# Kernel optimization log

Measured on AMD Instinct MI355X. Metric: run time of the kernel, lower is better.

Reference implementation:

```python
import jax, jax.numpy as jnp
import numpy as np

V_IPC, N_ROLES, D = 50000, 16, 256
B, L = 2048, 64
F_BIB, H1, H2, D_OUT = 512, 1024, 1024, 512
N_EXP, N_CLS = 8, 10
LN_EPS = 1e-5


def setup_inputs() -> dict:
    key = jax.random.key(0)
    ks = jax.random.split(key, 24)
    s = 0.05
    ipc_emb = jax.random.normal(ks[0], (V_IPC, D), jnp.float32) * s
    ipc_emb = ipc_emb.at[0].set(0.0)  # padding_idx=0
    role_emb = jax.random.normal(ks[1], (N_ROLES, D), jnp.float32) * s
    role_emb = role_emb.at[0].set(0.0)
    inp = {
        "ipc_indices": jax.random.randint(ks[2], (B, L), 0, V_IPC),
        "role_indices": jax.random.randint(ks[3], (B, L), 0, N_ROLES),
        "bibliometric_features": jax.random.normal(ks[4], (B, F_BIB), jnp.float32),
        "ipc_padding_mask": jax.random.randint(ks[5], (B, L), 0, 2).astype(jnp.int32),
        "top_k": 2,
        "ipc_emb": ipc_emb,
        "role_emb": role_emb,
        "Wq": jax.random.normal(ks[6], (D, D), jnp.float32) * s,
        "bq": jnp.zeros((D,), jnp.float32),
        "Wk": jax.random.normal(ks[7], (D, D), jnp.float32) * s,
        "bk": jnp.zeros((D,), jnp.float32),
        "Wv": jax.random.normal(ks[8], (D, D), jnp.float32) * s,
        "bv": jnp.zeros((D,), jnp.float32),
        "global_context": jax.random.normal(ks[9], (D,), jnp.float32) * s,
        "ln_g": jnp.ones((D,), jnp.float32),
        "ln_b": jnp.zeros((D,), jnp.float32),
        "gate_W": jax.random.normal(ks[10], (D, N_EXP), jnp.float32) * s,
        "gate_b": jnp.zeros((N_EXP,), jnp.float32),
        "expert_biases": jnp.zeros((N_EXP,), jnp.float32),
        "W1": jax.random.normal(ks[11], (N_EXP, F_BIB, H1), jnp.float32) * s,
        "b1": jnp.zeros((N_EXP, H1), jnp.float32),
        "W2": jax.random.normal(ks[12], (N_EXP, H1, H2), jnp.float32) * s,
        "b2": jnp.zeros((N_EXP, H2), jnp.float32),
        "W3": jax.random.normal(ks[13], (N_EXP, H2, D_OUT), jnp.float32) * s,
        "b3": jnp.zeros((N_EXP, D_OUT), jnp.float32),
        "head_W": jax.random.normal(ks[14], (D_OUT, N_CLS), jnp.float32) * s,
        "head_b": jnp.zeros((N_CLS,), jnp.float32),
    }
    return inp


def reference(ipc_indices, role_indices, bibliometric_features, ipc_padding_mask, top_k,
              ipc_emb, role_emb, Wq, bq, Wk, bk, Wv, bv, global_context, ln_g, ln_b,
              gate_W, gate_b, expert_biases, W1, b1, W2, b2, W3, b3, head_W, head_b):
    # embeddings + role combine  -> [B, L, D]
    x = ipc_emb[ipc_indices] + role_emb[role_indices]
    # attention pooling with a global learned query (same query for every batch row)
    keys = x @ Wk + bk                                  # [B, L, D]
    values = x @ Wv + bv                                # [B, L, D]
    q = global_context @ Wq + bq                        # [D]
    scores = jnp.einsum('d,bld->bl', q, keys)           # [B, L]
    scores = jnp.where(ipc_padding_mask == 0, -1e9, scores)
    attn = jax.nn.softmax(scores, axis=-1)              # [B, L]
    pooled = jnp.einsum('bl,bld->bd', attn, values)     # [B, D]
    mu = pooled.mean(-1, keepdims=True)
    var = ((pooled - mu) ** 2).mean(-1, keepdims=True)
    router_in = (pooled - mu) / jnp.sqrt(var + LN_EPS) * ln_g + ln_b
    # router: select with biased scores, gate with unbiased scores
    affinity = router_in @ gate_W + gate_b              # [B, E]
    sel_scores = affinity + expert_biases
    _, idx = jax.lax.top_k(sel_scores, top_k)           # [B, K]
    gw = jax.nn.softmax(jnp.take_along_axis(affinity, idx, axis=-1), axis=-1)  # [B, K]
    # dense all-expert MLP (reference form of masked per-expert loop)
    h = jax.nn.relu(jnp.einsum('bi,eih->ebh', bibliometric_features, W1) + b1[:, None, :])
    h = jax.nn.relu(jnp.einsum('ebh,ehj->ebj', h, W2) + b2[:, None, :])
    eo = jnp.einsum('ebj,ejo->ebo', h, W3) + b3[:, None, :]  # [E, B, O]
    # gather each token's top-k expert outputs and combine
    bidx = jnp.arange(idx.shape[0])[:, None]            # [B, 1]
    sel_out = eo[idx, bidx]                             # [B, K, O]
    moe_out = jnp.einsum('bk,bko->bo', gw, sel_out)     # [B, O]
    logits = moe_out @ head_W + head_b                  # [B, n_classes]
    return logits, idx
```

## Files before the change

### kernel.cpp

```cpp
#include <hip/hip_runtime.h>
#include <hip/hip_bf16.h>
#include <math.h>


#define LN_EPS 1e-5f

typedef __bf16 bf16_t;
typedef __bf16 bf16x8 __attribute__((ext_vector_type(8)));
typedef float f32x4 __attribute__((ext_vector_type(4)));

struct f4x2 { float4 a, b; };
__device__ __forceinline__ f4x2 ldA8(const float* p) {
  f4x2 v; v.a = *(const float4*)p; v.b = *(const float4*)(p + 4); return v;
}
__device__ __forceinline__ bf16x8 cvt8(const f4x2& v) {
  bf16x8 o;
  o[0] = (bf16_t)v.a.x; o[1] = (bf16_t)v.a.y; o[2] = (bf16_t)v.a.z; o[3] = (bf16_t)v.a.w;
  o[4] = (bf16_t)v.b.x; o[5] = (bf16_t)v.b.y; o[6] = (bf16_t)v.b.z; o[7] = (bf16_t)v.b.w;
  return o;
}

__global__ __launch_bounds__(256)
void prep_kq_kernel(const float* __restrict__ Wq, const float* __restrict__ bq,
                    const float* __restrict__ Wk, const float* __restrict__ bk,
                    const float* __restrict__ gc, float* __restrict__ kq_out) {
  __shared__ float q[256];
  __shared__ float red[4];
  const int t = threadIdx.x, bi = blockIdx.x;
  float s = bq[t];
  for (int d = 0; d < 256; d++) s += gc[d] * Wq[d * 256 + t];
  q[t] = s;
  __syncthreads();
  const int rl = t >> 5, sl = t & 31;
  const int r = bi * 8 + rl;
  float p = 0.f;
#pragma unroll
  for (int i = 0; i < 8; i++) { const int d = sl + 32 * i; p += Wk[r * 256 + d] * q[d]; }
#pragma unroll
  for (int o = 16; o > 0; o >>= 1) p += __shfl_down(p, o, 32);
  if (sl == 0) kq_out[r] = p;
  if (bi == 0) {
    float z2 = q[t] * bk[t];
    const int lane = t & 63, wave = t >> 6;
#pragma unroll
    for (int o = 32; o > 0; o >>= 1) z2 += __shfl_down(z2, o);
    if (lane == 0) red[wave] = z2;
    __syncthreads();
    if (t == 0) kq_out[256] = red[0] + red[1] + red[2] + red[3];
  }
}

__global__ __launch_bounds__(256)
void xbar_transpose(const float* __restrict__ W1, const float* __restrict__ W2,
                    const float* __restrict__ W3, bf16_t* __restrict__ B1,
                    bf16_t* __restrict__ B2, bf16_t* __restrict__ B3,
                    const int* __restrict__ ipc_idx, const int* __restrict__ role_idx,
                    const int* __restrict__ maskp,
                    const float* __restrict__ ipc_emb, const float* __restrict__ role_emb,
                    const float* __restrict__ kq_qbk, float* __restrict__ xbar_g) {
  __shared__ __align__(16) float smem[4480];
  const int bid = blockIdx.x;
  const int t = threadIdx.x, lane = t & 63;

  if (bid < 2048) {
    const int b = bid, wave = t >> 6;
    float* sred = smem;
    float* scores_s = smem + 4352;
    float* attn_s = smem + 4416;
    const float4 kq = *(const float4*)(kq_qbk + lane * 4);
    const float qbk = kq_qbk[256];
    const int rbase = b * 64 + wave * 16;
    int4 m4[4], i4[4], r4[4];
#pragma unroll
    for (int j = 0; j < 4; j++) {
      m4[j] = *(const int4*)(maskp + rbase + j * 4);
      i4[j] = *(const int4*)(ipc_idx + rbase + j * 4);
      r4[j] = *(const int4*)(role_idx + rbase + j * 4);
    }
#pragma unroll
    for (int i = 0; i < 16; i++) {
      const int mki = (&m4[i / 4].x)[i % 4];
      const int ii = mki ? (&i4[i / 4].x)[i % 4] : 0;
      const int ri = mki ? (&r4[i / 4].x)[i % 4] : 0;
      const float4 xe = *(const float4*)(ipc_emb + (size_t)ii * 256 + lane * 4);
      const float4 re = *(const float4*)(role_emb + (size_t)ri * 256 + lane * 4);
      sred[(wave * 64 + lane) * 17 + i] =
          (xe.x + re.x) * kq.x + (xe.y + re.y) * kq.y +
          (xe.z + re.z) * kq.z + (xe.w + re.w) * kq.w;
    }
    __syncthreads();
    {
      const int i_r = lane & 15, g = lane >> 4;
      float s = 0.f;
#pragma unroll
      for (int j = 0; j < 16; j++) s += sred[(wave * 64 + g * 16 + j) * 17 + i_r];
      s += __shfl_xor(s, 16);
      s += __shfl_xor(s, 32);
      const int mval = maskp[rbase + i_r];
      if (lane < 16) scores_s[wave * 16 + lane] = mval ? (s + qbk) : -1e9f;
    }
    __syncthreads();
    if (wave == 0) {
      const float sv = scores_s[lane];
      float m = sv;
#pragma unroll
      for (int o = 32; o > 0; o >>= 1) m = fmaxf(m, __shfl_xor(m, o));
      const float ev = expf(sv - m);
      float sum = ev;
#pragma unroll
      for (int o = 32; o > 0; o >>= 1) sum += __shfl_xor(sum, o);
      attn_s[lane] = ev / sum;
    }
    __syncthreads();
    float p0 = 0.f, p1 = 0.f, p2 = 0.f, p3 = 0.f;
#pragma unroll
    for (int i = 0; i < 16; i++) {
      const int mki = (&m4[i / 4].x)[i % 4];
      const int ii = mki ? (&i4[i / 4].x)[i % 4] : 0;
      const int ri = mki ? (&r4[i / 4].x)[i % 4] : 0;
      const float a = attn_s[wave * 16 + i];
      const float4 xe = *(const float4*)(ipc_emb + (size_t)ii * 256 + lane * 4);
      const float4 re = *(const float4*)(role_emb + (size_t)ri * 256 + lane * 4);
      p0 += a * (xe.x + re.x); p1 += a * (xe.y + re.y);
      p2 += a * (xe.z + re.z); p3 += a * (xe.w + re.w);
    }
    __syncthreads();
    *(float4*)&smem[wave * 256 + lane * 4] = make_float4(p0, p1, p2, p3);
    __syncthreads();
    xbar_g[(size_t)b * 256 + t] = smem[t] + smem[256 + t] + smem[512 + t] + smem[768 + t];
    return;
  }

  const int bid2 = bid - 2048;
  const float* W; bf16_t* Bft; int K, N, e, n0, k0;
  if (bid2 < 1024) {
    W = W1; Bft = B1; K = 512; N = 1024;
    e = bid2 >> 7; const int r = bid2 & 127;
    n0 = (r & 15) * 64; k0 = (r >> 4) * 64;
  } else if (bid2 < 3072) {
    W = W2; Bft = B2; K = 1024; N = 1024;
    const int q = bid2 - 1024; e = q >> 8; const int r = q & 255;
    n0 = (r & 15) * 64; k0 = (r >> 4) * 64;
  } else {
    W = W3; Bft = B3; K = 1024; N = 512;
    const int q = bid2 - 3072; e = q >> 7; const int r = q & 127;
    n0 = (r & 7) * 64; k0 = (r >> 3) * 64;
  }
  float (*tile)[65] = (float(*)[65])smem;
  const float* Wp = W + (size_t)e * K * N;
  bf16_t* Bp = Bft + (size_t)e * N * K;
  const int tq = t & 15, th = t >> 4;
#pragma unroll
  for (int i = 0; i < 4; i++) {
    const int row = th + 16 * i;
    *(float4*)&tile[row][tq * 4] = *(const float4*)(Wp + (size_t)(k0 + row) * N + n0 + tq * 4);
  }
  __syncthreads();
  const int sub = t >> 6;
  const int nk = K >> 5;
#pragma unroll
  for (int it = 0; it < 2; it++) {
    const int fid = sub + it * 4;
    const int ntl = fid & 3, ktl = fid >> 2;
    const int n_l = ntl * 16 + (lane & 15);
    const int k_l = ktl * 32 + (lane >> 4) * 8;
    bf16x8 o;
#pragma unroll
    for (int j = 0; j < 8; j++) o[j] = (bf16_t)tile[k_l + j][n_l];
    const size_t idx = ((((size_t)(n0 >> 4) + ntl) * nk + (k0 >> 5) + ktl) * 64 + lane) * 8;
    *(bf16x8*)(Bp + idx) = o;
  }
}

__global__ __launch_bounds__(256)
void pool_kernel(const float* __restrict__ xbar_g, const float* __restrict__ Wv,
                 const float* __restrict__ bvec,
                 const float* __restrict__ ln_g, const float* __restrict__ ln_b,
                 const float* __restrict__ gate_W, const float* __restrict__ gate_b,
                 const float* __restrict__ expert_biases,
                 float* __restrict__ out_idx_f, int* __restrict__ ws_idx,
                 float* __restrict__ ws_gw) {
  const int rb = blockIdx.x * 8;
  __shared__ __align__(16) float xs[8][256];
  __shared__ __align__(16) float pp[4][8][256];
  const int t = threadIdx.x, wave = t >> 6, lane = t & 63;
  for (int i = t; i < 512; i += 256)
    ((float4*)xs)[i] = ((const float4*)(xbar_g + (size_t)rb * 256))[i];
  __syncthreads();
  f32x4 acc[8];
#pragma unroll
  for (int r = 0; r < 8; r++) acc[r] = (f32x4){0.f, 0.f, 0.f, 0.f};
  const int dbase = wave * 64;
  for (int dd = 0; dd < 64; dd += 4) {
    float4 xr[8];
#pragma unroll
    for (int r = 0; r < 8; r++) xr[r] = *(const float4*)&xs[r][dbase + dd];
#pragma unroll
    for (int j = 0; j < 4; j++) {
      const float4 wv = *(const float4*)(Wv + (size_t)(dbase + dd + j) * 256 + lane * 4);
#pragma unroll
      for (int r = 0; r < 8; r++) {
        const float xv = (&xr[r].x)[j];
        acc[r][0] += xv * wv.x; acc[r][1] += xv * wv.y;
        acc[r][2] += xv * wv.z; acc[r][3] += xv * wv.w;
      }
    }
  }
#pragma unroll
  for (int r = 0; r < 8; r++) *(f32x4*)&pp[wave][r][lane * 4] = acc[r];
  __syncthreads();
  const float4 bvv = *(const float4*)(bvec + lane * 4);
  const float4 lg = *(const float4*)(ln_g + lane * 4);
  const float4 lb = *(const float4*)(ln_b + lane * 4);
#pragma unroll
  for (int rr = 0; rr < 2; rr++) {
    const int r = wave * 2 + rr;
    f32x4 v = *(const f32x4*)&pp[0][r][lane * 4];
#pragma unroll
    for (int w2 = 1; w2 < 4; w2++) {
      const f32x4 qv = *(const f32x4*)&pp[w2][r][lane * 4];
      v[0] += qv[0]; v[1] += qv[1]; v[2] += qv[2]; v[3] += qv[3];
    }
    v[0] += bvv.x; v[1] += bvv.y; v[2] += bvv.z; v[3] += bvv.w;
    float s1 = v[0] + v[1] + v[2] + v[3];
#pragma unroll
    for (int o = 32; o > 0; o >>= 1) s1 += __shfl_xor(s1, o);
    const float mu = s1 * (1.f / 256.f);
    const float4 df = make_float4(v[0] - mu, v[1] - mu, v[2] - mu, v[3] - mu);
    float s2 = df.x * df.x + df.y * df.y + df.z * df.z + df.w * df.w;
#pragma unroll
    for (int o = 32; o > 0; o >>= 1) s2 += __shfl_xor(s2, o);
    const float inv = 1.f / sqrtf(s2 * (1.f / 256.f) + LN_EPS);
    f32x4 rv;
    rv[0] = df.x * inv * lg.x + lb.x; rv[1] = df.y * inv * lg.y + lb.y;
    rv[2] = df.z * inv * lg.z + lb.z; rv[3] = df.w * inv * lg.w + lb.w;
    f32x4 pa = {0.f, 0.f, 0.f, 0.f}, pb = {0.f, 0.f, 0.f, 0.f};
#pragma unroll
    for (int k = 0; k < 4; k++) {
      const int d = lane * 4 + k;
      const f32x4 g0 = *(const f32x4*)(gate_W + d * 8);
      const f32x4 g1 = *(const f32x4*)(gate_W + d * 8 + 4);
      pa += rv[k] * g0;
      pb += rv[k] * g1;
    }
#pragma unroll
    for (int o = 32; o > 0; o >>= 1) {
      pa[0] += __shfl_down(pa[0], o); pa[1] += __shfl_down(pa[1], o);
      pa[2] += __shfl_down(pa[2], o); pa[3] += __shfl_down(pa[3], o);
      pb[0] += __shfl_down(pb[0], o); pb[1] += __shfl_down(pb[1], o);
      pb[2] += __shfl_down(pb[2], o); pb[3] += __shfl_down(pb[3], o);
    }
    if (lane == 0) {
      float aff[8];
#pragma unroll
      for (int j = 0; j < 4; j++) { aff[j] = pa[j] + gate_b[j]; aff[4 + j] = pb[j] + gate_b[4 + j]; }
      float b0 = -1e30f; int i0 = 0;
#pragma unroll
      for (int j = 0; j < 8; j++) {
        const float s = aff[j] + expert_biases[j];
        if (s > b0) { b0 = s; i0 = j; }
      }
      float b1v = -1e30f; int i1 = 0;
#pragma unroll
      for (int j = 0; j < 8; j++) {
        const float s = aff[j] + expert_biases[j];
        if (j != i0 && s > b1v) { b1v = s; i1 = j; }
      }
      const float a0 = aff[i0], a1 = aff[i1];
      const float m = fmaxf(a0, a1);
      const float e0 = expf(a0 - m), e1 = expf(a1 - m);
      const float invs = 1.f / (e0 + e1);
      const int bg = rb + r;
      ws_idx[bg * 2] = i0; ws_idx[bg * 2 + 1] = i1;
      ws_gw[bg * 2] = e0 * invs; ws_gw[bg * 2 + 1] = e1 * invs;
      out_idx_f[bg * 2] = (float)i0; out_idx_f[bg * 2 + 1] = (float)i1;
    }
  }
}

__global__ __launch_bounds__(256)
void pack_kernel(const int* __restrict__ ws_idx, int* __restrict__ list_token,
                 int* __restrict__ a_of, int* __restrict__ offsets_g) {
  __shared__ int cnt[8]; __shared__ int off[9]; __shared__ int fill[8];
  const int t = threadIdx.x;
  if (t < 8) cnt[t] = 0;
  __syncthreads();
  for (int a = t; a < 4096; a += 256) atomicAdd(&cnt[ws_idx[a]], 1);
  __syncthreads();
  if (t == 0) {
    off[0] = 0;
    for (int e = 0; e < 8; e++) off[e + 1] = off[e] + ((cnt[e] + 63) & ~63);
  }
  __syncthreads();
  if (t < 8) fill[t] = off[t];
  if (t < 9) offsets_g[t] = off[t];
  for (int a = t; a < 4608; a += 256) list_token[a] = 0;
  __syncthreads();
  for (int a = t; a < 4096; a += 256) {
    const int e = ws_idx[a];
    const int pos = atomicAdd(&fill[e], 1);
    list_token[pos] = a >> 1;
    a_of[a] = pos;
  }
}

template <int NT, bool RELU>
__global__ __launch_bounds__(256)
void expert_gemm_g1(const float* __restrict__ bib, const int* __restrict__ list_token,
                    const bf16_t* __restrict__ Bft, const float* __restrict__ bias,
                    bf16_t* __restrict__ C, const int* __restrict__ offsets) {
  constexpr int K = 512, nk = K / 32;
  const int e = blockIdx.z;
  const int seg_hi = offsets[e + 1];
  const int blk_row = offsets[e] + blockIdx.y * 128;
  if (blk_row >= seg_hi) return;
  const int wave = threadIdx.x >> 6, lane = threadIdx.x & 63;
  const int row0 = blk_row + wave * 32;
  if (row0 >= seg_hi) return;
  const int n0 = blockIdx.x * 64;
  const int tok0 = list_token[row0 + (lane & 15)];
  const int tok1 = list_token[row0 + 16 + (lane & 15)];
  const float* Ap0 = bib + (size_t)tok0 * 512 + (lane >> 4) * 8;
  const float* Ap1 = bib + (size_t)tok1 * 512 + (lane >> 4) * 8;
  const bf16_t* Bp = Bft + (size_t)e * NT * K + ((size_t)(n0 >> 4) * nk * 512 + lane * 8);
  f32x4 acc[2][4];
#pragma unroll
  for (int i = 0; i < 2; i++)
#pragma unroll
    for (int j = 0; j < 4; j++) acc[i][j] = (f32x4){0.f, 0.f, 0.f, 0.f};
  f4x2 aS[2][2]; bf16x8 bX[2][4];
  aS[0][0] = ldA8(Ap0); aS[0][1] = ldA8(Ap1);
#pragma unroll
  for (int ni = 0; ni < 4; ni++) bX[0][ni] = *(const bf16x8*)(Bp + (size_t)ni * nk * 512);
#pragma unroll
  for (int kt = 0; kt < nk; kt++) {
    const int cur = kt & 1, nxt = cur ^ 1;
    if (kt + 1 < nk) {
      aS[nxt][0] = ldA8(Ap0 + (kt + 1) * 32);
      aS[nxt][1] = ldA8(Ap1 + (kt + 1) * 32);
#pragma unroll
      for (int ni = 0; ni < 4; ni++)
        bX[nxt][ni] = *(const bf16x8*)(Bp + ((size_t)ni * nk + kt + 1) * 512);
    }
    const bf16x8 a0 = cvt8(aS[cur][0]), a1 = cvt8(aS[cur][1]);
#pragma unroll
    for (int ni = 0; ni < 4; ni++) {
      acc[0][ni] = __builtin_amdgcn_mfma_f32_16x16x32_bf16(a0, bX[cur][ni], acc[0][ni], 0, 0, 0);
      acc[1][ni] = __builtin_amdgcn_mfma_f32_16x16x32_bf16(a1, bX[cur][ni], acc[1][ni], 0, 0, 0);
    }
  }
  const int fr = lane & 15, q = lane >> 4;
#pragma unroll
  for (int ni = 0; ni < 4; ni++) {
    const int col = n0 + ni * 16 + fr;
    const float bv = bias[e * NT + col];
#pragma unroll
    for (int mi = 0; mi < 2; mi++) {
#pragma unroll
      for (int r = 0; r < 4; r++) {
        const int row = row0 + mi * 16 + q * 4 + r;
        float v = acc[mi][ni][r] + bv;
        if (RELU) v = fmaxf(v, 0.f);
        C[(size_t)row * NT + col] = (bf16_t)v;
      }
    }
  }
}

template <int K, int NT, bool RELU, typename OUT_T>
__global__ __launch_bounds__(256)
void expert_gemm_ft(const bf16_t* __restrict__ A, const bf16_t* __restrict__ Bft,
                    const float* __restrict__ bias, OUT_T* __restrict__ C,
                    const int* __restrict__ offsets) {
  constexpr int nk = K / 32;
  const int e = blockIdx.z;
  const int seg_hi = offsets[e + 1];
  const int blk_row = offsets[e] + blockIdx.y * 128;
  if (blk_row >= seg_hi) return;
  const int wave = threadIdx.x >> 6, lane = threadIdx.x & 63;
  const int row0 = blk_row + wave * 32;
  if (row0 >= seg_hi) return;
  const int n0 = blockIdx.x * 64;
  const bf16_t* Ap = A + (size_t)(row0 + (lane & 15)) * K + ((lane >> 4) * 8);
  const bf16_t* Bp = Bft + (size_t)e * NT * K + ((size_t)(n0 >> 4) * nk * 512 + lane * 8);
  f32x4 acc[2][4];
#pragma unroll
  for (int i = 0; i < 2; i++)
#pragma unroll
    for (int j = 0; j < 4; j++) acc[i][j] = (f32x4){0.f, 0.f, 0.f, 0.f};
  bf16x8 aX[2][2], bX[2][4];
#pragma unroll
  for (int mi = 0; mi < 2; mi++) aX[0][mi] = *(const bf16x8*)(Ap + mi * 16 * K);
#pragma unroll
  for (int ni = 0; ni < 4; ni++) bX[0][ni] = *(const bf16x8*)(Bp + (size_t)ni * nk * 512);
#pragma unroll
  for (int kt = 0; kt < nk; kt++) {
    const int cur = kt & 1, nxt = cur ^ 1;
    if (kt + 1 < nk) {
#pragma unroll
      for (int mi = 0; mi < 2; mi++)
        aX[nxt][mi] = *(const bf16x8*)(Ap + mi * 16 * K + (kt + 1) * 32);
#pragma unroll
      for (int ni = 0; ni < 4; ni++)
        bX[nxt][ni] = *(const bf16x8*)(Bp + ((size_t)ni * nk + kt + 1) * 512);
    }
#pragma unroll
    for (int mi = 0; mi < 2; mi++)
#pragma unroll
      for (int ni = 0; ni < 4; ni++)
        acc[mi][ni] = __builtin_amdgcn_mfma_f32_16x16x32_bf16(aX[cur][mi], bX[cur][ni], acc[mi][ni], 0, 0, 0);
  }
  const int fr = lane & 15, q = lane >> 4;
#pragma unroll
  for (int ni = 0; ni < 4; ni++) {
    const int col = n0 + ni * 16 + fr;
    const float bv = bias[e * NT + col];
#pragma unroll
    for (int mi = 0; mi < 2; mi++) {
#pragma unroll
      for (int r = 0; r < 4; r++) {
        const int row = row0 + mi * 16 + q * 4 + r;
        float v = acc[mi][ni][r] + bv;
        if (RELU) v = fmaxf(v, 0.f);
        C[(size_t)row * NT + col] = (OUT_T)v;
      }
    }
  }
}

__global__ __launch_bounds__(256)
void head_kernel(const float* __restrict__ O, const int* __restrict__ a_of,
                 const float* __restrict__ ws_gw, const float* __restrict__ head_W,
                 const float* __restrict__ head_b, float* __restrict__ out) {
  const int b = blockIdx.x, t = threadIdx.x;
  __shared__ float m[512];
  const int a0 = a_of[b * 2], a1 = a_of[b * 2 + 1];
  const float g0 = ws_gw[b * 2], g1 = ws_gw[b * 2 + 1];
  for (int d = t; d < 512; d += 256)
    m[d] = g0 * O[(size_t)a0 * 512 + d] + g1 * O[(size_t)a1 * 512 + d];
  __syncthreads();
  if (t < 160) {
    const int c = t >> 4, ch = t & 15;
    float p = 0.f;
#pragma unroll
    for (int i = 0; i < 32; i++) {
      const int d = i * 16 + ch;
      p += m[d] * head_W[d * 10 + c];
    }
#pragma unroll
    for (int o = 8; o > 0; o >>= 1) p += __shfl_down(p, o, 16);
    if (ch == 0) out[b * 10 + c] = p + head_b[c];
  }
}

extern "C" void kernel_launch(void* const* d_in, const int* in_sizes, int n_in,
                              void* d_out, int out_size, void* d_ws, size_t ws_size,
                              hipStream_t stream) {
  const int* ipc_idx = (const int*)d_in[0];
  const int* role_idx = (const int*)d_in[1];
  const float* bib = (const float*)d_in[2];
  const int* maskp = (const int*)d_in[3];
  const float* ipc_emb = (const float*)d_in[5];
  const float* role_emb = (const float*)d_in[6];
  const float* Wq = (const float*)d_in[7];
  const float* bq = (const float*)d_in[8];
  const float* Wk = (const float*)d_in[9];
  const float* bk = (const float*)d_in[10];
  const float* Wv = (const float*)d_in[11];
  const float* bv = (const float*)d_in[12];
  const float* gc = (const float*)d_in[13];
  const float* ln_g = (const float*)d_in[14];
  const float* ln_b = (const float*)d_in[15];
  const float* gate_W = (const float*)d_in[16];
  const float* gate_b = (const float*)d_in[17];
  const float* exp_b = (const float*)d_in[18];
  const float* W1 = (const float*)d_in[19];
  const float* b1 = (const float*)d_in[20];
  const float* W2 = (const float*)d_in[21];
  const float* b2 = (const float*)d_in[22];
  const float* W3 = (const float*)d_in[23];
  const float* b3 = (const float*)d_in[24];
  const float* head_W = (const float*)d_in[25];
  const float* head_b = (const float*)d_in[26];

  char* ws = (char*)d_ws;
  size_t off = 0;
  auto alloc = [&](size_t bytes) -> char* {
    char* p = ws + off;
    off += (bytes + 255) & ~(size_t)255;
    return p;
  };
  float* kq_qbk = (float*)alloc(257 * 4);
  float* xbar_g = (float*)alloc((size_t)2048 * 256 * 4);
  int* ws_idx = (int*)alloc(4096 * 4);
  float* ws_gw = (float*)alloc(4096 * 4);
  int* list_tok = (int*)alloc(4608 * 4);
  int* a_of = (int*)alloc(4096 * 4);
  int* offs = (int*)alloc(9 * 4);
  bf16_t* W1t = (bf16_t*)alloc((size_t)8 * 1024 * 512 * 2);
  bf16_t* W2t = (bf16_t*)alloc((size_t)8 * 1024 * 1024 * 2);
  bf16_t* W3t = (bf16_t*)alloc((size_t)8 * 512 * 1024 * 2);
  bf16_t* H1c = (bf16_t*)alloc((size_t)4608 * 1024 * 2);
  bf16_t* H2c = (bf16_t*)alloc((size_t)4608 * 1024 * 2);
  float* Oc = (float*)alloc((size_t)4608 * 512 * 4);
  (void)in_sizes; (void)n_in; (void)out_size; (void)ws_size;

  float* out_logits = (float*)d_out;
  float* out_idx = (float*)d_out + 20480;

  prep_kq_kernel<<<32, 256, 0, stream>>>(Wq, bq, Wk, bk, gc, kq_qbk);
  xbar_transpose<<<6144, 256, 0, stream>>>(W1, W2, W3, W1t, W2t, W3t,
                                           ipc_idx, role_idx, maskp,
                                           ipc_emb, role_emb, kq_qbk, xbar_g);
  pool_kernel<<<256, 256, 0, stream>>>(xbar_g, Wv, bv, ln_g, ln_b, gate_W, gate_b,
                                       exp_b, out_idx, ws_idx, ws_gw);
  pack_kernel<<<1, 256, 0, stream>>>(ws_idx, list_tok, a_of, offs);
  expert_gemm_g1<1024, true><<<dim3(16, 36, 8), 256, 0, stream>>>(bib, list_tok, W1t, b1, H1c, offs);
  expert_gemm_ft<1024, 1024, true, bf16_t><<<dim3(16, 36, 8), 256, 0, stream>>>(H1c, W2t, b2, H2c, offs);
  expert_gemm_ft<1024, 512, false, float><<<dim3(8, 36, 8), 256, 0, stream>>>(H2c, W3t, b3, Oc, offs);
  head_kernel<<<2048, 256, 0, stream>>>(Oc, a_of, ws_gw, head_W, head_b, out_logits);
}
```

Baseline: 356.3 us.

## Fuse pack into pool via last-block counter, stage indices in LDS

The single-block pack kernel is folded into pool_kernel: each block bumps a global done counter, and the last block to finish performs the expert counting and list packing. This removes one kernel launch and its dependency gap. The counter is reset in prep_kq_kernel. In xbar_transpose, mask and index loads now go through shared memory once per block instead of per-wave int4 register loads. A launch bounds occupancy hint of 8 is also added, which may constrain registers.

```diff
diff --git a/kernel.cpp b/kernel.cpp
--- a/kernel.cpp
+++ b/kernel.cpp
@@ -23,10 +23,12 @@
 __global__ __launch_bounds__(256)
 void prep_kq_kernel(const float* __restrict__ Wq, const float* __restrict__ bq,
                     const float* __restrict__ Wk, const float* __restrict__ bk,
-                    const float* __restrict__ gc, float* __restrict__ kq_out) {
+                    const float* __restrict__ gc, float* __restrict__ kq_out,
+                    int* __restrict__ done_ctr) {
   __shared__ float q[256];
   __shared__ float red[4];
   const int t = threadIdx.x, bi = blockIdx.x;
+  if (bi == 0 && t == 0) *done_ctr = 0;
   float s = bq[t];
   for (int d = 0; d < 256; d++) s += gc[d] * Wq[d * 256 + t];
   q[t] = s;
@@ -50,7 +52,7 @@
   }
 }
 
-__global__ __launch_bounds__(256)
+__global__ __launch_bounds__(256, 8)
 void xbar_transpose(const float* __restrict__ W1, const float* __restrict__ W2,
                     const float* __restrict__ W3, bf16_t* __restrict__ B1,
                     bf16_t* __restrict__ B2, bf16_t* __restrict__ B3,
@@ -59,6 +61,7 @@
                     const float* __restrict__ ipc_emb, const float* __restrict__ role_emb,
                     const float* __restrict__ kq_qbk, float* __restrict__ xbar_g) {
   __shared__ __align__(16) float smem[4480];
+  __shared__ int s_ii[64], s_ri[64], s_mk[64];
   const int bid = blockIdx.x;
   const int t = threadIdx.x, lane = t & 63;
 
@@ -69,19 +72,17 @@
     float* attn_s = smem + 4416;
     const float4 kq = *(const float4*)(kq_qbk + lane * 4);
     const float qbk = kq_qbk[256];
-    const int rbase = b * 64 + wave * 16;
-    int4 m4[4], i4[4], r4[4];
-#pragma unroll
-    for (int j = 0; j < 4; j++) {
-      m4[j] = *(const int4*)(maskp + rbase + j * 4);
-      i4[j] = *(const int4*)(ipc_idx + rbase + j * 4);
-      r4[j] = *(const int4*)(role_idx + rbase + j * 4);
-    }
+    if (t < 64) {
+      const int mk = maskp[b * 64 + t];
+      s_mk[t] = mk;
+      s_ii[t] = mk ? ipc_idx[b * 64 + t] : 0;
+      s_ri[t] = mk ? role_idx[b * 64 + t] : 0;
+    }
+    __syncthreads();
 #pragma unroll
     for (int i = 0; i < 16; i++) {
-      const int mki = (&m4[i / 4].x)[i % 4];
-      const int ii = mki ? (&i4[i / 4].x)[i % 4] : 0;
-      const int ri = mki ? (&r4[i / 4].x)[i % 4] : 0;
+      const int row = wave * 16 + i;
+      const int ii = s_ii[row], ri = s_ri[row];
       const float4 xe = *(const float4*)(ipc_emb + (size_t)ii * 256 + lane * 4);
       const float4 re = *(const float4*)(role_emb + (size_t)ri * 256 + lane * 4);
       sred[(wave * 64 + lane) * 17 + i] =
@@ -96,8 +97,8 @@
       for (int j = 0; j < 16; j++) s += sred[(wave * 64 + g * 16 + j) * 17 + i_r];
       s += __shfl_xor(s, 16);
       s += __shfl_xor(s, 32);
-      const int mval = maskp[rbase + i_r];
-      if (lane < 16) scores_s[wave * 16 + lane] = mval ? (s + qbk) : -1e9f;
+      if (lane < 16)
+        scores_s[wave * 16 + lane] = s_mk[wave * 16 + lane] ? (s + qbk) : -1e9f;
     }
     __syncthreads();
     if (wave == 0) {
@@ -115,10 +116,9 @@
     float p0 = 0.f, p1 = 0.f, p2 = 0.f, p3 = 0.f;
 #pragma unroll
     for (int i = 0; i < 16; i++) {
-      const int mki = (&m4[i / 4].x)[i % 4];
-      const int ii = mki ? (&i4[i / 4].x)[i % 4] : 0;
-      const int ri = mki ? (&r4[i / 4].x)[i % 4] : 0;
-      const float a = attn_s[wave * 16 + i];
+      const int row = wave * 16 + i;
+      const int ii = s_ii[row], ri = s_ri[row];
+      const float a = attn_s[row];
       const float4 xe = *(const float4*)(ipc_emb + (size_t)ii * 256 + lane * 4);
       const float4 re = *(const float4*)(role_emb + (size_t)ri * 256 + lane * 4);
       p0 += a * (xe.x + re.x); p1 += a * (xe.y + re.y);
@@ -179,10 +179,13 @@
                  const float* __restrict__ gate_W, const float* __restrict__ gate_b,
                  const float* __restrict__ expert_biases,
                  float* __restrict__ out_idx_f, int* __restrict__ ws_idx,
-                 float* __restrict__ ws_gw) {
+                 float* __restrict__ ws_gw, int* __restrict__ done_ctr,
+                 int* __restrict__ list_token, int* __restrict__ a_of,
+                 int* __restrict__ offsets_g) {
   const int rb = blockIdx.x * 8;
   __shared__ __align__(16) float xs[8][256];
   __shared__ __align__(16) float pp[4][8][256];
+  __shared__ int is_last;
   const int t = threadIdx.x, wave = t >> 6, lane = t & 63;
   for (int i = t; i < 512; i += 256)
     ((float4*)xs)[i] = ((const float4*)(xbar_g + (size_t)rb * 256))[i];
@@ -276,31 +279,35 @@
       out_idx_f[bg * 2] = (float)i0; out_idx_f[bg * 2 + 1] = (float)i1;
     }
   }
-}
-
-__global__ __launch_bounds__(256)
-void pack_kernel(const int* __restrict__ ws_idx, int* __restrict__ list_token,
-                 int* __restrict__ a_of, int* __restrict__ offsets_g) {
-  __shared__ int cnt[8]; __shared__ int off[9]; __shared__ int fill[8];
-  const int t = threadIdx.x;
-  if (t < 8) cnt[t] = 0;
-  __syncthreads();
-  for (int a = t; a < 4096; a += 256) atomicAdd(&cnt[ws_idx[a]], 1);
   __syncthreads();
   if (t == 0) {
-    off[0] = 0;
-    for (int e = 0; e < 8; e++) off[e + 1] = off[e] + ((cnt[e] + 63) & ~63);
-  }
-  __syncthreads();
-  if (t < 8) fill[t] = off[t];
-  if (t < 9) offsets_g[t] = off[t];
-  for (int a = t; a < 4608; a += 256) list_token[a] = 0;
-  __syncthreads();
-  for (int a = t; a < 4096; a += 256) {
-    const int e = ws_idx[a];
-    const int pos = atomicAdd(&fill[e], 1);
-    list_token[pos] = a >> 1;
-    a_of[a] = pos;
+    __threadfence();
+    const int prev = atomicAdd(done_ctr, 1);
+    is_last = (prev == (int)gridDim.x - 1);
+  }
+  __syncthreads();
+  if (is_last) {
+    __threadfence();
+    __shared__ int cnt[8]; __shared__ int offp[9]; __shared__ int fill[8];
+    if (t < 8) cnt[t] = 0;
+    __syncthreads();
+    for (int a = t; a < 4096; a += 256) atomicAdd(&cnt[ws_idx[a]], 1);
+    __syncthreads();
+    if (t == 0) {
+      offp[0] = 0;
+      for (int e = 0; e < 8; e++) offp[e + 1] = offp[e] + ((cnt[e] + 63) & ~63);
+    }
+    __syncthreads();
+    if (t < 8) fill[t] = offp[t];
+    if (t < 9) offsets_g[t] = offp[t];
+    for (int a = t; a < 4608; a += 256) list_token[a] = 0;
+    __syncthreads();
+    for (int a = t; a < 4096; a += 256) {
+      const int e = ws_idx[a];
+      const int pos = atomicAdd(&fill[e], 1);
+      list_token[pos] = a >> 1;
+      a_of[a] = pos;
+    }
   }
 }
 
@@ -497,6 +504,7 @@
   int* list_tok = (int*)alloc(4608 * 4);
   int* a_of = (int*)alloc(4096 * 4);
   int* offs = (int*)alloc(9 * 4);
+  int* done_ctr = (int*)alloc(4);
   bf16_t* W1t = (bf16_t*)alloc((size_t)8 * 1024 * 512 * 2);
   bf16_t* W2t = (bf16_t*)alloc((size_t)8 * 1024 * 1024 * 2);
   bf16_t* W3t = (bf16_t*)alloc((size_t)8 * 512 * 1024 * 2);
@@ -508,13 +516,13 @@
   float* out_logits = (float*)d_out;
   float* out_idx = (float*)d_out + 20480;
 
-  prep_kq_kernel<<<32, 256, 0, stream>>>(Wq, bq, Wk, bk, gc, kq_qbk);
+  prep_kq_kernel<<<32, 256, 0, stream>>>(Wq, bq, Wk, bk, gc, kq_qbk, done_ctr);
   xbar_transpose<<<6144, 256, 0, stream>>>(W1, W2, W3, W1t, W2t, W3t,
                                            ipc_idx, role_idx, maskp,
                                            ipc_emb, role_emb, kq_qbk, xbar_g);
   pool_kernel<<<256, 256, 0, stream>>>(xbar_g, Wv, bv, ln_g, ln_b, gate_W, gate_b,
-                                       exp_b, out_idx, ws_idx, ws_gw);
-  pack_kernel<<<1, 256, 0, stream>>>(ws_idx, list_tok, a_of, offs);
+                                       exp_b, out_idx, ws_idx, ws_gw,
+                                       done_ctr, list_tok, a_of, offs);
   expert_gemm_g1<1024, true><<<dim3(16, 36, 8), 256, 0, stream>>>(bib, list_tok, W1t, b1, H1c, offs);
   expert_gemm_ft<1024, 1024, true, bf16_t><<<dim3(16, 36, 8), 256, 0, stream>>>(H1c, W2t, b2, H2c, offs);
   expert_gemm_ft<1024, 512, false, float><<<dim3(8, 36, 8), 256, 0, stream>>>(H2c, W3t, b3, Oc, offs);
```

After: 365.8 us. 2.7% more time.
